# Performance work log

Hardware: AMD Instinct MI355X
Metric: run time of the kernel (lower is better)

Reference implementation:

```python
import jax, jax.numpy as jnp
import numpy as np

B, T, C = 4, 2048, 1024
E, F, K = 8, 2048, 2


def setup_inputs() -> dict:
    key = jax.random.key(0)
    k0, k1, k2, k3 = jax.random.split(key, 4)
    s = lambda d: 1.0 / np.sqrt(d)
    x = jax.random.normal(k0, (B, T, C), dtype=jnp.float32)
    Wr = jax.random.normal(k1, (E, C), dtype=jnp.float32) * s(C)      # router: nn.Linear(C, E) weight [E, C]
    W1 = jax.random.normal(k2, (E, 2 * F, C), dtype=jnp.float32) * s(C)  # per-expert w1 [2F, C]
    W2 = jax.random.normal(k3, (E, C, F), dtype=jnp.float32) * s(F)      # per-expert w2 [C, F]
    return {"x": x, "Wr": Wr, "W1": W1, "W2": W2}


def reference(x, Wr, W1, W2):
    Bb, Tt, Cc = x.shape
    flat = x.reshape(-1, Cc)                         # [N, C]
    N = flat.shape[0]
    # router: top-k then softmax over the k selected logits
    logits = flat @ Wr.T                             # [N, E]
    weights, ids = jax.lax.top_k(logits, K)          # [N, K]
    weights = jax.nn.softmax(weights, axis=-1)
    rows = jnp.arange(N)[:, None]
    router_weights = jnp.zeros((N, E), dtype=flat.dtype).at[rows, ids].add(weights)  # [N, E]
    # all experts on all tokens (dense reference), SwiGLU
    h = jnp.einsum('nc,efc->nef', flat, W1)          # [N, E, 2F]
    val, gate = h[..., :F], h[..., F:]
    act = val * jax.nn.silu(gate)                    # [N, E, F]
    expert_outputs = jnp.einsum('nef,ecf->nec', act, W2)  # [N, E, C]
    out = jnp.einsum('nec,ne->nc', expert_outputs, router_weights)
    return out.reshape(Bb, Tt, Cc)
```

## Files before the change

kernel.cpp:

```cpp
#include <hip/hip_runtime.h>

#define NTOK 8192
#define CDIM 1024
#define FDIM 2048
#define NEXP 8
#define CAP  16384
#define NPAIR 16384
#define MTCAP 32

typedef __bf16 bf16x8 __attribute__((ext_vector_type(8)));
typedef float  f32x4  __attribute__((ext_vector_type(4)));

__device__ __forceinline__ unsigned short f2bf(float f) {
    unsigned int u = __builtin_bit_cast(unsigned int, f);
    unsigned int r = (u + 0x7FFFu + ((u >> 16) & 1u)) >> 16;
    return (unsigned short)r;
}

__device__ __forceinline__ unsigned int pack2(float lo, float hi) {
    return ((unsigned int)f2bf(hi) << 16) | (unsigned int)f2bf(lo);
}

__device__ __forceinline__ float bflo(unsigned int u) {
    return __builtin_bit_cast(float, u << 16);
}
__device__ __forceinline__ float bfhi(unsigned int u) {
    return __builtin_bit_cast(float, u & 0xFFFF0000u);
}

__device__ __forceinline__ void gload_lds16(const void* g, void* l) {
    __builtin_amdgcn_global_load_lds(
        (const __attribute__((address_space(1))) unsigned int*)g,
        (__attribute__((address_space(3))) unsigned int*)l, 16, 0, 0);
}

#define BARRIER() asm volatile("s_barrier" ::: "memory")
#define WAIT_LGKM0() do { asm volatile("s_waitcnt lgkmcnt(0)" ::: "memory"); __builtin_amdgcn_sched_barrier(0); } while (0)
#define WAITVM0() asm volatile("s_waitcnt vmcnt(0)" ::: "memory")

__global__ void cvt_kernel(const float* __restrict__ s, unsigned short* __restrict__ d, long ngrp) {
    long i = (long)blockIdx.x * blockDim.x + threadIdx.x;
    long stride = (long)gridDim.x * blockDim.x;
    const float4* s4 = (const float4*)s;
    uint4* d4 = (uint4*)d;
    for (long g = i; g < ngrp; g += stride) {
        float4 a = s4[2 * g], b = s4[2 * g + 1];
        uint4 o;
        o.x = pack2(a.x, a.y); o.y = pack2(a.z, a.w);
        o.z = pack2(b.x, b.y); o.w = pack2(b.z, b.w);
        d4[g] = o;
    }
}

__global__ __launch_bounds__(256) void logits_kernel(
    const float* __restrict__ x, const float* __restrict__ Wr,
    float* __restrict__ wgt, int* __restrict__ eids)
{
    int w = threadIdx.x >> 6, l = threadIdx.x & 63;
    int t = blockIdx.x * 4 + w;
    const float* xr = x + (size_t)t * CDIM;
    float acc[NEXP];
    #pragma unroll
    for (int e = 0; e < NEXP; e++) acc[e] = 0.f;
    for (int c = l; c < CDIM; c += 64) {
        float xv = xr[c];
        #pragma unroll
        for (int e = 0; e < NEXP; e++) acc[e] += xv * Wr[e * CDIM + c];
    }
    #pragma unroll
    for (int e = 0; e < NEXP; e++)
        for (int off = 32; off > 0; off >>= 1) acc[e] += __shfl_down(acc[e], off);
    if (l == 0) {
        int i0 = 0; float l0 = acc[0];
        #pragma unroll
        for (int e = 1; e < NEXP; e++) if (acc[e] > l0) { l0 = acc[e]; i0 = e; }
        int i1 = -1; float l1 = -3.4e38f;
        #pragma unroll
        for (int e = 0; e < NEXP; e++) if (e != i0 && acc[e] > l1) { l1 = acc[e]; i1 = e; }
        float tv = __expf(l1 - l0);
        float den = 1.f + tv;
        wgt[2 * t] = 1.f / den;
        wgt[2 * t + 1] = tv / den;
        eids[t] = i0 | (i1 << 8);
    }
}

__global__ __launch_bounds__(256) void bucket_kernel(
    const int* __restrict__ eids, int* __restrict__ list, int* __restrict__ cnt)
{
    __shared__ int lcnt[NEXP];
    __shared__ int lbase[NEXP];
    int t = threadIdx.x;
    if (t < NEXP) lcnt[t] = 0;
    __syncthreads();
    int tok = blockIdx.x * 256 + t;
    int id = eids[tok];
    int e0 = id & 0xff, e1 = (id >> 8) & 0xff;
    int s0 = atomicAdd(&lcnt[e0], 1);
    int s1 = atomicAdd(&lcnt[e1], 1);
    __syncthreads();
    if (t < NEXP) lbase[t] = atomicAdd(&cnt[t], lcnt[t]);
    __syncthreads();
    list[e0 * CAP + lbase[e0] + s0] = 2 * tok;
    list[e1 * CAP + lbase[e1] + s1] = 2 * tok + 1;
}

__global__ void offs_kernel(const int* __restrict__ cnt, int* __restrict__ offs) {
    if (threadIdx.x == 0) {
        int a = 0;
        for (int e = 0; e < NEXP; e++) { offs[e] = a; a += cnt[e]; }
    }
}

__global__ __launch_bounds__(256) void pack_kernel(
    const float* __restrict__ x, const int* __restrict__ list,
    const int* __restrict__ cnt, const int* __restrict__ offs,
    const float* __restrict__ wgt,
    unsigned short* __restrict__ xg, float* __restrict__ wgs)
{
    int e = blockIdx.y;
    int cnt_e = cnt[e];
    int s0 = blockIdx.x * 16;
    if (s0 >= cnt_e) return;
    int t = threadIdx.x;
    int sr = s0 + (t >> 4);
    if (sr >= cnt_e) return;
    int p = list[e * CAP + sr];
    int tok = p >> 1;
    if ((t & 15) == 0) wgs[offs[e] + sr] = wgt[p];
    const float4* src = (const float4*)(x + (size_t)tok * CDIM);
    uint2* dst = (uint2*)(xg + (size_t)(offs[e] + sr) * CDIM);
    int c = t & 15;
    #pragma unroll
    for (int i = 0; i < 16; i++) {
        float4 v = src[c + i * 16];
        uint2 o; o.x = pack2(v.x, v.y); o.y = pack2(v.z, v.w);
        dst[c + i * 16] = o;
    }
}

__global__ __launch_bounds__(256, 2) void gemm1_kernel(
    const unsigned short* __restrict__ xg,
    const unsigned short* __restrict__ W1b,
    const float* __restrict__ wgs,
    unsigned short* __restrict__ act,
    const int* __restrict__ cnt, const int* __restrict__ offs)
{
    int e = blockIdx.z, nt = blockIdx.x, mt = blockIdx.y;
    int cnt_e = cnt[e];
    if (mt * 128 >= cnt_e) return;
    int off_e = offs[e];

    __shared__ __align__(16) char lds[32768];

    int t = threadIdx.x, l = t & 63, w = t >> 6;
    int wave_m = w >> 1, wave_n = w & 1;

    int c2s = ((t & 3) * 16) ^ (((t >> 5) & 1) << 5);
    int dst = t * 16;

    const char *sA0, *sA1, *sBv, *sBg;
    {
        int r0 = min(mt * 128 + (t >> 2), cnt_e - 1);
        int r1 = min(mt * 128 + 64 + (t >> 2), cnt_e - 1);
        sA0 = (const char*)xg + (size_t)(off_e + r0) * 2048 + c2s;
        sA1 = (const char*)xg + (size_t)(off_e + r1) * 2048 + c2s;
        int f = nt * 64 + (t >> 2);
        sBv = (const char*)W1b + ((size_t)e * 2 * FDIM + f) * 2048 + c2s;
        sBg = sBv + (size_t)FDIM * 2048;
    }

    int lane_off = (l & 15) * 64 + (((l >> 4) * 16) ^ (((l >> 3) & 1) << 5));
    f32x4 accV[4][2] = {}, accG[4][2] = {};

#define G1_STAGE(KB) do { \
        gload_lds16(sA0 + (KB),      (char*)lds + dst); \
        gload_lds16(sA1 + (KB),      (char*)lds + 4096 + dst); \
        gload_lds16(sA0 + (KB) + 64, (char*)lds + 8192 + dst); \
        gload_lds16(sA1 + (KB) + 64, (char*)lds + 12288 + dst); \
        gload_lds16(sBv + (KB),      (char*)lds + 16384 + dst); \
        gload_lds16(sBv + (KB) + 64, (char*)lds + 20480 + dst); \
        gload_lds16(sBg + (KB),      (char*)lds + 24576 + dst); \
        gload_lds16(sBg + (KB) + 64, (char*)lds + 28672 + dst); \
    } while (0)

    G1_STAGE(0);

    #pragma unroll
    for (int kt = 0; kt < 16; kt++) {
        WAITVM0();
        BARRIER();

        bf16x8 af[2][4], bv[2][2], bg[2][2];
        #pragma unroll
        for (int h = 0; h < 2; h++) {
            #pragma unroll
            for (int m = 0; m < 4; m++)
                af[h][m] = *(const bf16x8*)((char*)lds + h * 8192 + (wave_m * 4 + m) * 1024 + lane_off);
            #pragma unroll
            for (int n = 0; n < 2; n++) {
                bv[h][n] = *(const bf16x8*)((char*)lds + 16384 + h * 4096 + (wave_n * 2 + n) * 1024 + lane_off);
                bg[h][n] = *(const bf16x8*)((char*)lds + 24576 + h * 4096 + (wave_n * 2 + n) * 1024 + lane_off);
            }
        }
        WAIT_LGKM0();
        BARRIER();

        if (kt != 15) { int kb = (kt + 1) * 128; G1_STAGE(kb); }
        __builtin_amdgcn_sched_barrier(0);

        __builtin_amdgcn_s_setprio(1);
        #pragma unroll
        for (int h = 0; h < 2; h++)
            #pragma unroll
            for (int m = 0; m < 4; m++)
                #pragma unroll
                for (int n = 0; n < 2; n++) {
                    accV[m][n] = __builtin_amdgcn_mfma_f32_16x16x32_bf16(af[h][m], bv[h][n], accV[m][n], 0, 0, 0);
                    accG[m][n] = __builtin_amdgcn_mfma_f32_16x16x32_bf16(af[h][m], bg[h][n], accG[m][n], 0, 0, 0);
                }
        __builtin_amdgcn_s_setprio(0);
    }
#undef G1_STAGE

    int colF = nt * 64 + wave_n * 32 + (l & 15);
    int rowB = mt * 128 + wave_m * 64 + ((l >> 4) * 4);
    #pragma unroll
    for (int m = 0; m < 4; m++) {
        #pragma unroll
        for (int r = 0; r < 4; r++) {
            int srow = rowB + m * 16 + r;
            if (srow < cnt_e) {
                float wsc = wgs[off_e + srow];
                #pragma unroll
                for (int n = 0; n < 2; n++) {
                    float g = accG[m][n][r];
                    float v = accV[m][n][r];
                    float aa = wsc * v * g / (1.f + __expf(-g));
                    act[(size_t)(off_e + srow) * FDIM + colF + n * 16] = f2bf(aa);
                }
            }
        }
    }
}

__global__ __launch_bounds__(256, 2) void gemm2_kernel(
    const unsigned short* __restrict__ act,
    const unsigned short* __restrict__ W2b,
    const int* __restrict__ list, const int* __restrict__ cnt,
    const int* __restrict__ offs,
    unsigned short* __restrict__ eob)
{
    int e = blockIdx.z, nt = blockIdx.x, mt = blockIdx.y;
    int cnt_e = cnt[e];
    if (mt * 128 >= cnt_e) return;
    int off_e = offs[e];
    const int* le = list + e * CAP;

    __shared__ __align__(16) char lds[32768];

    int t = threadIdx.x, l = t & 63, w = t >> 6;
    int wave_m = w >> 1, wave_n = w & 1;

    int c2s = ((t & 3) * 16) ^ (((t >> 5) & 1) << 5);
    int dst = t * 16;

    const char *sA0, *sA1, *sB0, *sB1;
    {
        int r0 = min(mt * 128 + (t >> 2), cnt_e - 1);
        int r1 = min(mt * 128 + 64 + (t >> 2), cnt_e - 1);
        sA0 = (const char*)act + (size_t)(off_e + r0) * 4096 + c2s;
        sA1 = (const char*)act + (size_t)(off_e + r1) * 4096 + c2s;
        int c0 = nt * 128 + (t >> 2);
        sB0 = (const char*)W2b + ((size_t)e * CDIM + c0) * 4096 + c2s;
        sB1 = sB0 + (size_t)64 * 4096;
    }

    int lane_off = (l & 15) * 64 + (((l >> 4) * 16) ^ (((l >> 3) & 1) << 5));
    f32x4 acc[4][4] = {};

#define G2_STAGE(KB) do { \
        gload_lds16(sA0 + (KB),      (char*)lds + dst); \
        gload_lds16(sA1 + (KB),      (char*)lds + 4096 + dst); \
        gload_lds16(sA0 + (KB) + 64, (char*)lds + 8192 + dst); \
        gload_lds16(sA1 + (KB) + 64, (char*)lds + 12288 + dst); \
        gload_lds16(sB0 + (KB),      (char*)lds + 16384 + dst); \
        gload_lds16(sB1 + (KB),      (char*)lds + 20480 + dst); \
        gload_lds16(sB0 + (KB) + 64, (char*)lds + 24576 + dst); \
        gload_lds16(sB1 + (KB) + 64, (char*)lds + 28672 + dst); \
    } while (0)

    G2_STAGE(0);

    #pragma unroll
    for (int kt = 0; kt < 32; kt++) {
        WAITVM0();
        BARRIER();

        bf16x8 af[2][4], bf[2][4];
        #pragma unroll
        for (int h = 0; h < 2; h++) {
            #pragma unroll
            for (int m = 0; m < 4; m++)
                af[h][m] = *(const bf16x8*)((char*)lds + h * 8192 + (wave_m * 4 + m) * 1024 + lane_off);
            #pragma unroll
            for (int n = 0; n < 4; n++)
                bf[h][n] = *(const bf16x8*)((char*)lds + 16384 + h * 8192 + (wave_n * 4 + n) * 1024 + lane_off);
        }
        WAIT_LGKM0();
        BARRIER();

        if (kt != 31) { int kb = (kt + 1) * 128; G2_STAGE(kb); }
        __builtin_amdgcn_sched_barrier(0);

        __builtin_amdgcn_s_setprio(1);
        #pragma unroll
        for (int h = 0; h < 2; h++)
            #pragma unroll
            for (int m = 0; m < 4; m++)
                #pragma unroll
                for (int n = 0; n < 4; n++)
                    acc[m][n] = __builtin_amdgcn_mfma_f32_16x16x32_bf16(af[h][m], bf[h][n], acc[m][n], 0, 0, 0);
        __builtin_amdgcn_s_setprio(0);
    }
#undef G2_STAGE

    int colC = nt * 128 + wave_n * 64 + (l & 15);
    int rowB = mt * 128 + wave_m * 64 + ((l >> 4) * 4);
    #pragma unroll
    for (int m = 0; m < 4; m++) {
        #pragma unroll
        for (int r = 0; r < 4; r++) {
            int srow = rowB + m * 16 + r;
            if (srow < cnt_e) {
                int p = le[srow];
                #pragma unroll
                for (int n = 0; n < 4; n++)
                    eob[(size_t)p * CDIM + colC + n * 16] = f2bf(acc[m][n][r]);
            }
        }
    }
}

__global__ __launch_bounds__(256) void combine_kernel(
    const unsigned short* __restrict__ eob, float* __restrict__ out)
{
    const long NG = (long)NTOK * (CDIM / 4);
    long i = (long)blockIdx.x * blockDim.x + threadIdx.x;
    long stride = (long)gridDim.x * blockDim.x;
    float4* out4 = (float4*)out;
    for (long g = i; g < NG; g += stride) {
        long t = g >> 8;
        long j = g & 255;
        uint2 a = ((const uint2*)(eob + (size_t)(2 * t) * CDIM))[j];
        uint2 b = ((const uint2*)(eob + (size_t)(2 * t + 1) * CDIM))[j];
        float4 o;
        o.x = bflo(a.x) + bflo(b.x);
        o.y = bfhi(a.x) + bfhi(b.x);
        o.z = bflo(a.y) + bflo(b.y);
        o.w = bfhi(a.y) + bfhi(b.y);
        out4[g] = o;
    }
}

extern "C" void kernel_launch(void* const* d_in, const int* in_sizes, int n_in,
                              void* d_out, int out_size, void* d_ws, size_t ws_size,
                              hipStream_t stream) {
    const float* x  = (const float*)d_in[0];
    const float* Wr = (const float*)d_in[1];
    const float* W1 = (const float*)d_in[2];
    const float* W2 = (const float*)d_in[3];
    float* out = (float*)d_out;
    char* ws = (char*)d_ws;

    const size_t OFF_XG   = 0;
    const size_t OFF_W1B  = OFF_XG  + (size_t)NPAIR * CDIM * 2;
    const size_t OFF_ACT  = OFF_W1B + (size_t)NEXP * 2 * FDIM * CDIM * 2;
    const size_t OFF_LIST = OFF_ACT + (size_t)NPAIR * FDIM * 2;
    const size_t OFF_WGT  = OFF_LIST + (size_t)NEXP * CAP * 4;
    const size_t OFF_WGS  = OFF_WGT + (size_t)NPAIR * 4;
    const size_t OFF_CNT  = OFF_WGS + (size_t)NPAIR * 4;
    const size_t OFF_OFFS = OFF_CNT + 32;
    const size_t OFF_EIDS = OFF_OFFS + 32;

    unsigned short* xg  = (unsigned short*)(ws + OFF_XG);
    unsigned short* W1b = (unsigned short*)(ws + OFF_W1B);
    unsigned short* act = (unsigned short*)(ws + OFF_ACT);
    int*   list = (int*)(ws + OFF_LIST);
    float* wgt  = (float*)(ws + OFF_WGT);
    float* wgs  = (float*)(ws + OFF_WGS);
    int*   cnt  = (int*)(ws + OFF_CNT);
    int*   offs = (int*)(ws + OFF_OFFS);
    int*   eids = (int*)(ws + OFF_EIDS);
    unsigned short* W2b = (unsigned short*)(ws + OFF_W1B);
    unsigned short* eob = (unsigned short*)(ws + OFF_XG);

    hipMemsetAsync(cnt, 0, NEXP * sizeof(int), stream);

    cvt_kernel<<<4096, 256, 0, stream>>>(W1, W1b, (long)NEXP * 2 * FDIM * CDIM / 8);
    logits_kernel<<<NTOK / 4, 256, 0, stream>>>(x, Wr, wgt, eids);
    bucket_kernel<<<NTOK / 256, 256, 0, stream>>>(eids, list, cnt);
    offs_kernel<<<1, 64, 0, stream>>>(cnt, offs);
    pack_kernel<<<dim3(256, NEXP), 256, 0, stream>>>(x, list, cnt, offs, wgt, xg, wgs);

    gemm1_kernel<<<dim3(FDIM / 64, MTCAP, NEXP), 256, 0, stream>>>(xg, W1b, wgs, act, cnt, offs);

    cvt_kernel<<<4096, 256, 0, stream>>>(W2, W2b, (long)NEXP * CDIM * FDIM / 8);

    gemm2_kernel<<<dim3(CDIM / 128, MTCAP, NEXP), 256, 0, stream>>>(act, W2b, list, cnt, offs, eob);
    combine_kernel<<<2048, 256, 0, stream>>>(eob, out);
}
```

Measured before the change: 357.9 us.

## Split gemm2 K dimension in two halves and vectorize router and pack loads

The second expert GEMM now splits its K=2048 reduction into two halves across twice as many blocks. Each half writes to its own bf16 partial buffer, and the combine kernel sums the two partials per expert pair. The aim is more parallelism and better occupancy in gemm2, whose grid was small when per-expert token counts are uneven. The router logits kernel and the pack kernel also switch to wider float4/uint4 loads and stores. The costs are an extra partial buffer write and read, and an extra bf16 rounding step on the partial sums.

Result: no change. 352.8 us (-1.4%).

```diff
diff --git a/kernel.cpp b/kernel.cpp
--- a/kernel.cpp
+++ b/kernel.cpp
@@ -58,14 +58,20 @@
 {
     int w = threadIdx.x >> 6, l = threadIdx.x & 63;
     int t = blockIdx.x * 4 + w;
-    const float* xr = x + (size_t)t * CDIM;
+    const float4* xr = (const float4*)(x + (size_t)t * CDIM);
+    const float4* Wr4 = (const float4*)Wr;
     float acc[NEXP];
     #pragma unroll
     for (int e = 0; e < NEXP; e++) acc[e] = 0.f;
-    for (int c = l; c < CDIM; c += 64) {
-        float xv = xr[c];
-        #pragma unroll
-        for (int e = 0; e < NEXP; e++) acc[e] += xv * Wr[e * CDIM + c];
+    #pragma unroll
+    for (int i = 0; i < 4; i++) {
+        int idx = l + 64 * i;
+        float4 xv = xr[idx];
+        #pragma unroll
+        for (int e = 0; e < NEXP; e++) {
+            float4 wv = Wr4[e * 256 + idx];
+            acc[e] += xv.x * wv.x + xv.y * wv.y + xv.z * wv.z + xv.w * wv.w;
+        }
     }
     #pragma unroll
     for (int e = 0; e < NEXP; e++)
@@ -129,12 +135,15 @@
     int tok = p >> 1;
     if ((t & 15) == 0) wgs[offs[e] + sr] = wgt[p];
     const float4* src = (const float4*)(x + (size_t)tok * CDIM);
-    uint2* dst = (uint2*)(xg + (size_t)(offs[e] + sr) * CDIM);
+    uint4* dst = (uint4*)(xg + (size_t)(offs[e] + sr) * CDIM);
     int c = t & 15;
     #pragma unroll
-    for (int i = 0; i < 16; i++) {
-        float4 v = src[c + i * 16];
-        uint2 o; o.x = pack2(v.x, v.y); o.y = pack2(v.z, v.w);
+    for (int i = 0; i < 8; i++) {
+        float4 a = src[2 * c + i * 32];
+        float4 b = src[2 * c + 1 + i * 32];
+        uint4 o;
+        o.x = pack2(a.x, a.y); o.y = pack2(a.z, a.w);
+        o.z = pack2(b.x, b.y); o.w = pack2(b.z, b.w);
         dst[c + i * 16] = o;
     }
 }
@@ -249,9 +258,11 @@
     const unsigned short* __restrict__ W2b,
     const int* __restrict__ list, const int* __restrict__ cnt,
     const int* __restrict__ offs,
-    unsigned short* __restrict__ eob)
-{
-    int e = blockIdx.z, nt = blockIdx.x, mt = blockIdx.y;
+    unsigned short* __restrict__ eob0,
+    unsigned short* __restrict__ eob1)
+{
+    int e = blockIdx.z, mt = blockIdx.y;
+    int nt = blockIdx.x & 7, kh = blockIdx.x >> 3;
     int cnt_e = cnt[e];
     if (mt * 128 >= cnt_e) return;
     int off_e = offs[e];
@@ -269,10 +280,11 @@
     {
         int r0 = min(mt * 128 + (t >> 2), cnt_e - 1);
         int r1 = min(mt * 128 + 64 + (t >> 2), cnt_e - 1);
-        sA0 = (const char*)act + (size_t)(off_e + r0) * 4096 + c2s;
-        sA1 = (const char*)act + (size_t)(off_e + r1) * 4096 + c2s;
+        size_t khb = (size_t)kh * 2048;
+        sA0 = (const char*)act + (size_t)(off_e + r0) * 4096 + khb + c2s;
+        sA1 = (const char*)act + (size_t)(off_e + r1) * 4096 + khb + c2s;
         int c0 = nt * 128 + (t >> 2);
-        sB0 = (const char*)W2b + ((size_t)e * CDIM + c0) * 4096 + c2s;
+        sB0 = (const char*)W2b + ((size_t)e * CDIM + c0) * 4096 + khb + c2s;
         sB1 = sB0 + (size_t)64 * 4096;
     }
 
@@ -293,7 +305,7 @@
     G2_STAGE(0);
 
     #pragma unroll
-    for (int kt = 0; kt < 32; kt++) {
+    for (int kt = 0; kt < 16; kt++) {
         WAITVM0();
         BARRIER();
 
@@ -310,7 +322,7 @@
         WAIT_LGKM0();
         BARRIER();
 
-        if (kt != 31) { int kb = (kt + 1) * 128; G2_STAGE(kb); }
+        if (kt != 15) { int kb = (kt + 1) * 128; G2_STAGE(kb); }
         __builtin_amdgcn_sched_barrier(0);
 
         __builtin_amdgcn_s_setprio(1);
@@ -325,6 +337,7 @@
     }
 #undef G2_STAGE
 
+    unsigned short* eob = kh ? eob1 : eob0;
     int colC = nt * 128 + wave_n * 64 + (l & 15);
     int rowB = mt * 128 + wave_m * 64 + ((l >> 4) * 4);
     #pragma unroll
@@ -343,7 +356,8 @@
 }
 
 __global__ __launch_bounds__(256) void combine_kernel(
-    const unsigned short* __restrict__ eob, float* __restrict__ out)
+    const unsigned short* __restrict__ eob0, const unsigned short* __restrict__ eob1,
+    float* __restrict__ out)
 {
     const long NG = (long)NTOK * (CDIM / 4);
     long i = (long)blockIdx.x * blockDim.x + threadIdx.x;
@@ -352,13 +366,15 @@
     for (long g = i; g < NG; g += stride) {
         long t = g >> 8;
         long j = g & 255;
-        uint2 a = ((const uint2*)(eob + (size_t)(2 * t) * CDIM))[j];
-        uint2 b = ((const uint2*)(eob + (size_t)(2 * t + 1) * CDIM))[j];
+        uint2 a0 = ((const uint2*)(eob0 + (size_t)(2 * t) * CDIM))[j];
+        uint2 b0 = ((const uint2*)(eob0 + (size_t)(2 * t + 1) * CDIM))[j];
+        uint2 a1 = ((const uint2*)(eob1 + (size_t)(2 * t) * CDIM))[j];
+        uint2 b1 = ((const uint2*)(eob1 + (size_t)(2 * t + 1) * CDIM))[j];
         float4 o;
-        o.x = bflo(a.x) + bflo(b.x);
-        o.y = bfhi(a.x) + bfhi(b.x);
-        o.z = bflo(a.y) + bflo(b.y);
-        o.w = bfhi(a.y) + bfhi(b.y);
+        o.x = (bflo(a0.x) + bflo(a1.x)) + (bflo(b0.x) + bflo(b1.x));
+        o.y = (bfhi(a0.x) + bfhi(a1.x)) + (bfhi(b0.x) + bfhi(b1.x));
+        o.z = (bflo(a0.y) + bflo(a1.y)) + (bflo(b0.y) + bflo(b1.y));
+        o.w = (bfhi(a0.y) + bfhi(a1.y)) + (bfhi(b0.y) + bfhi(b1.y));
         out4[g] = o;
     }
 }
@@ -392,8 +408,9 @@
     int*   cnt  = (int*)(ws + OFF_CNT);
     int*   offs = (int*)(ws + OFF_OFFS);
     int*   eids = (int*)(ws + OFF_EIDS);
-    unsigned short* W2b = (unsigned short*)(ws + OFF_W1B);
-    unsigned short* eob = (unsigned short*)(ws + OFF_XG);
+    unsigned short* W2b  = (unsigned short*)(ws + OFF_W1B);
+    unsigned short* eob1 = (unsigned short*)(ws + OFF_W1B + (size_t)NPAIR * CDIM * 2);
+    unsigned short* eob0 = (unsigned short*)(ws + OFF_XG);
 
     hipMemsetAsync(cnt, 0, NEXP * sizeof(int), stream);
 
@@ -407,6 +424,6 @@
 
     cvt_kernel<<<4096, 256, 0, stream>>>(W2, W2b, (long)NEXP * CDIM * FDIM / 8);
 
-    gemm2_kernel<<<dim3(CDIM / 128, MTCAP, NEXP), 256, 0, stream>>>(act, W2b, list, cnt, offs, eob);
-    combine_kernel<<<2048, 256, 0, stream>>>(eob, out);
-}
+    gemm2_kernel<<<dim3(16, MTCAP, NEXP), 256, 0, stream>>>(act, W2b, list, cnt, offs, eob0, eob1);
+    combine_kernel<<<2048, 256, 0, stream>>>(eob0, eob1, out);
+}
```
